# Kernel optimization log

Hardware: AMD Instinct MI355X
Metric: run time of the kernel (lower is better)

The kernel has to match this reference:

```python
import jax, jax.numpy as jnp
import numpy as np
import math

NUM_HEADS = 4
NUM_GROUPS = 16
EPS = 1e-5


def setup_inputs() -> dict:
    key = jax.random.key(0)
    ks = jax.random.split(key, 4)
    C = 256
    x = jax.random.normal(ks[0], (1, C, 16, 16, 16), dtype=jnp.float32)
    gn_gamma = jnp.ones((C,), dtype=jnp.float32)
    gn_beta = jnp.zeros((C,), dtype=jnp.float32)
    # conv3d 1x1 kernels == plain matrices [out_ch, in_ch]
    w_qkv = jax.random.normal(ks[1], (3 * C, C), dtype=jnp.float32) * (1.0 / math.sqrt(C))
    w_proj = jax.random.normal(ks[2], (C, C), dtype=jnp.float32) * (1.0 / math.sqrt(C))
    b_proj = jnp.zeros((C,), dtype=jnp.float32)
    return {"x": x, "gn_gamma": gn_gamma, "gn_beta": gn_beta,
            "w_qkv": w_qkv, "w_proj": w_proj, "b_proj": b_proj}


def reference(x, gn_gamma, gn_beta, w_qkv, w_proj, b_proj):
    B, C, H, W, D = x.shape
    N = H * W * D
    heads = NUM_HEADS
    d = C // heads

    xf = x.reshape(B, C, N)  # [B, C, N]

    # GroupNorm(16, C) with affine params
    xg = xf.reshape(B, NUM_GROUPS, C // NUM_GROUPS, N)
    mu = jnp.mean(xg, axis=(2, 3), keepdims=True)
    var = jnp.var(xg, axis=(2, 3), keepdims=True)
    xn = ((xg - mu) * jax.lax.rsqrt(var + EPS)).reshape(B, C, N)
    xn = xn * gn_gamma[None, :, None] + gn_beta[None, :, None]

    # 1x1 conv QKV: [B, 3C, N]
    qkv = jnp.einsum('oc,bcn->bon', w_qkv, xn)
    # torch: qkv.reshape(B*heads, 3d, N).chunk(3, dim=1)
    qkv = qkv.reshape(B * heads, 3 * d, N)
    q, k, v = qkv[:, :d], qkv[:, d:2 * d], qkv[:, 2 * d:]

    scale = 1.0 / math.sqrt(math.sqrt(d))
    attn = jnp.einsum('bct,bcs->bts', q * scale, k * scale)  # [B*heads, N, N]
    attn = jax.nn.softmax(attn, axis=-1)
    h = jnp.einsum('bts,bcs->bct', attn, v)  # [B*heads, d, N]

    h = h.reshape(B, C, N)
    out = jnp.einsum('oc,bcn->bon', w_proj, h) + b_proj[None, :, None]
    return (out + xf).reshape(B, C, H, W, D)
```

## Files before the change

kernel.cpp:

```cpp
#include <hip/hip_runtime.h>
#include <math.h>

#define N_TOK 4096
#define C_CH  256
#define SPLITS 4

typedef short bf16x8 __attribute__((ext_vector_type(8)));
typedef float f32x4  __attribute__((ext_vector_type(4)));
typedef unsigned short u16;

__device__ __forceinline__ u16 f2bf(float f) {
    union { float f; unsigned u; } v; v.f = f;
    unsigned r = v.u + 0x7FFF + ((v.u >> 16) & 1);
    return (u16)(r >> 16);
}
__device__ __forceinline__ float bf2f(u16 b) {
    union { unsigned u; float f; } v; v.u = ((unsigned)b) << 16;
    return v.f;
}
__device__ __forceinline__ unsigned packtr(float a, float b) {
    union { float f; unsigned u; } ua, ub; ua.f = a; ub.f = b;
    return __builtin_amdgcn_perm(ub.u, ua.u, 0x07060302u);
}

__global__ __launch_bounds__(256) void prep(const float* __restrict__ wqkv,
                                            const float* __restrict__ wproj,
                                            const float* __restrict__ x,
                                            u16* __restrict__ wq, u16* __restrict__ wp,
                                            float2* __restrict__ part) {
    __shared__ float rs[4], rss[4];
    if (blockIdx.x < 1024) {
        int i = blockIdx.x * 256 + threadIdx.x;
        if (i < 196608) {
            int row = i >> 8;
            float s = ((row % 192) < 64) ? 0.18033688f : 1.0f;
            wq[i] = f2bf(wqkv[i] * s);
        } else {
            wp[i - 196608] = f2bf(wproj[i - 196608]);
        }
    } else {
        const int b = blockIdx.x - 1024, tid = threadIdx.x;
        const int lane = tid & 63, wave = tid >> 6;
        const float4* xp = (const float4*)x + b * 1024;
        float s = 0.f, ss = 0.f;
#pragma unroll
        for (int k = 0; k < 4; ++k) {
            float4 v = xp[tid + k * 256];
            s  += v.x + v.y + v.z + v.w;
            ss += v.x * v.x + v.y * v.y + v.z * v.z + v.w * v.w;
        }
#pragma unroll
        for (int off = 1; off < 64; off <<= 1) {
            s  += __shfl_xor(s, off, 64);
            ss += __shfl_xor(ss, off, 64);
        }
        if (lane == 0) { rs[wave] = s; rss[wave] = ss; }
        __syncthreads();
        if (tid == 0) part[b] = make_float2(rs[0]+rs[1]+rs[2]+rs[3], rss[0]+rss[1]+rss[2]+rss[3]);
    }
}

__global__ __launch_bounds__(256) void qkv_gemm(const u16* __restrict__ wq,
                                                const float* __restrict__ x,
                                                const float2* __restrict__ part,
                                                const float* __restrict__ gamma,
                                                const float* __restrict__ beta,
                                                u16* __restrict__ QT,
                                                u16* __restrict__ KTm,
                                                u16* __restrict__ Vc) {
    const int nb = blockIdx.x * 64;
    const int tid = threadIdx.x;
    const int wave = tid >> 6, lane = tid & 63;
    const int quad = lane >> 4, low = lane & 15;
    const int mo = blockIdx.y * 64 + wave * 16;

    __shared__ __align__(16) u16 Xs[64 * 256];
    __shared__ float sca[256], scb[256];

    {
        const int ch = tid, g = ch >> 4;
        float s = 0.f, ss = 0.f;
#pragma unroll
        for (int j = 0; j < 16; ++j) { float2 p = part[g * 16 + j]; s += p.x; ss += p.y; }
        float mu = s * (1.f / 65536.f);
        float var = ss * (1.f / 65536.f) - mu * mu;
        float a = rsqrtf(var + 1e-5f) * gamma[ch];
        sca[ch] = a; scb[ch] = beta[ch] - mu * a;
    }
    __syncthreads();

#pragma unroll
    for (int i = 0; i < 8; ++i) {
        const int g = wave * 8 + i;
        u16 pk[8];
#pragma unroll
        for (int j = 0; j < 8; ++j) {
            const int ch = g * 8 + j;
            pk[j] = f2bf(x[ch * N_TOK + nb + lane] * sca[ch] + scb[ch]);
        }
        *(uint4*)(Xs + lane * 256 + ((g ^ (lane & 7)) * 8)) = *(const uint4*)pk;
    }
    __syncthreads();

    f32x4 acc[4] = {f32x4{0,0,0,0}, f32x4{0,0,0,0}, f32x4{0,0,0,0}, f32x4{0,0,0,0}};
#pragma unroll
    for (int kc = 0; kc < 8; ++kc) {
        bf16x8 af = *(const bf16x8*)(wq + (mo + low) * 256 + kc * 32 + quad * 8);
#pragma unroll
        for (int nt = 0; nt < 4; ++nt) {
            bf16x8 bf_ = *(const bf16x8*)(Xs + (nt * 16 + low) * 256 +
                                          (((kc * 4 + quad) ^ (low & 7)) * 8));
            acc[nt] = __builtin_amdgcn_mfma_f32_16x16x32_bf16(af, bf_, acc[nt], 0, 0, 0);
        }
    }

    const int kind = blockIdx.y % 3;
    const int head = blockIdx.y / 3;
    const int crow = wave * 16 + quad * 4;

    if (kind < 2) {
        u16* dst = (kind == 0 ? QT : KTm) + head * (N_TOK * 64);
#pragma unroll
        for (int nt = 0; nt < 4; ++nt) {
            int tok = nb + nt * 16 + low;
            u16 q4[4];
#pragma unroll
            for (int r = 0; r < 4; ++r) q4[r] = f2bf(acc[nt][r]);
            *(uint2*)(dst + tok * 64 + crow) = *(const uint2*)q4;
        }
    } else {
        __syncthreads();
        u16* Ts = Xs;
#pragma unroll
        for (int nt = 0; nt < 4; ++nt) {
            int tokl = nt * 16 + low;
#pragma unroll
            for (int r = 0; r < 4; ++r)
                Ts[(crow + r) * 72 + tokl] = f2bf(acc[nt][r]);
        }
        __syncthreads();
        u16* dst = Vc + head * (64 * N_TOK) + nb;
#pragma unroll
        for (int i = 0; i < 2; ++i) {
            int idx = i * 256 + tid;
            int c = idx >> 3, ch = idx & 7;
            uint4 v = *(const uint4*)(Ts + c * 72 + ch * 8);
            *(uint4*)(dst + c * N_TOK + ch * 8) = v;
        }
    }
}

__global__ __launch_bounds__(256, 2) void attn_kernel(const u16* __restrict__ QT,
                                                      const u16* __restrict__ KTm,
                                                      const u16* __restrict__ Vc,
                                                      u16* __restrict__ Op,
                                                      float* __restrict__ Lp) {
    const int head = blockIdx.y, split = blockIdx.z;
    const int qb   = blockIdx.x * 128;
    const int tid  = threadIdx.x;
    const int wave = tid >> 6, lane = tid & 63;
    const int quad = lane >> 4, low = lane & 15;

    const u16* Qh = QT  + head * N_TOK * 64;
    const u16* Kh = KTm + head * N_TOK * 64 + split * 1024 * 64;
    const u16* Vh = Vc  + head * 64 * N_TOK + split * 1024;

    __shared__ u16 Ks[2][64 * 64];
    __shared__ u16 Vs[2][64 * 64];
    __shared__ u16 Ps[4 * 32 * 64];
    u16* Pw = Ps + wave * 2048;

    bf16x8 ones;
#pragma unroll
    for (int i = 0; i < 8; ++i) ones[i] = (short)0x3F80;

    bf16x8 bq[2][2];
#pragma unroll
    for (int tn = 0; tn < 2; ++tn)
#pragma unroll
        for (int kh = 0; kh < 2; ++kh)
            bq[tn][kh] = *(const bf16x8*)(Qh + (qb + wave * 32 + tn * 16 + low) * 64 + kh * 32 + quad * 8);

    f32x4 oa[2][4], lC[2];
#pragma unroll
    for (int mt = 0; mt < 2; ++mt) {
        lC[mt] = f32x4{0,0,0,0};
#pragma unroll
        for (int cn = 0; cn < 4; ++cn) oa[mt][cn] = f32x4{0,0,0,0};
    }

    const int sA = tid >> 3, gA = tid & 7;
    const int swA = ((gA ^ (sA & 7)) * 8);
    const int swB = ((gA ^ ((sA + 32) & 7)) * 8);
    uint4 pk0 = *(const uint4*)(Kh + sA * 64 + gA * 8);
    uint4 pk1 = *(const uint4*)(Kh + (sA + 32) * 64 + gA * 8);
    uint4 pv0 = *(const uint4*)(Vh + sA * N_TOK + gA * 8);
    uint4 pv1 = *(const uint4*)(Vh + (sA + 32) * N_TOK + gA * 8);
    *(uint4*)(Ks[0] + sA * 64 + swA) = pk0;
    *(uint4*)(Ks[0] + (sA + 32) * 64 + swB) = pk1;
    *(uint4*)(Vs[0] + sA * 64 + swA) = pv0;
    *(uint4*)(Vs[0] + (sA + 32) * 64 + swB) = pv1;
    pk0 = *(const uint4*)(Kh + (64 + sA) * 64 + gA * 8);
    pk1 = *(const uint4*)(Kh + (64 + sA + 32) * 64 + gA * 8);
    pv0 = *(const uint4*)(Vh + sA * N_TOK + 64 + gA * 8);
    pv1 = *(const uint4*)(Vh + (sA + 32) * N_TOK + 64 + gA * 8);

    const int low7 = low & 7;

    for (int kt = 0; kt < 16; ++kt) {
        const int cur = kt & 1;
        const u16* Kc = Ks[cur];
        const u16* Vu = Vs[cur];
        __syncthreads();
        if (kt < 15) {
            u16* Kn = Ks[cur ^ 1]; u16* Vn = Vs[cur ^ 1];
            *(uint4*)(Kn + sA * 64 + swA) = pk0;
            *(uint4*)(Kn + (sA + 32) * 64 + swB) = pk1;
            *(uint4*)(Vn + sA * 64 + swA) = pv0;
            *(uint4*)(Vn + (sA + 32) * 64 + swB) = pv1;
            if (kt < 14) {
                int sb2 = (kt + 2) * 64;
                pk0 = *(const uint4*)(Kh + (sb2 + sA) * 64 + gA * 8);
                pk1 = *(const uint4*)(Kh + (sb2 + sA + 32) * 64 + gA * 8);
                pv0 = *(const uint4*)(Vh + sA * N_TOK + sb2 + gA * 8);
                pv1 = *(const uint4*)(Vh + (sA + 32) * N_TOK + sb2 + gA * 8);
            }
        }

        f32x4 sa[4][2];
#pragma unroll
        for (int sm = 0; sm < 4; ++sm)
#pragma unroll
            for (int tn = 0; tn < 2; ++tn) sa[sm][tn] = f32x4{0,0,0,0};
#pragma unroll
        for (int kh = 0; kh < 2; ++kh)
#pragma unroll
            for (int sm = 0; sm < 4; ++sm) {
                bf16x8 ak = *(const bf16x8*)(Kc + (sm * 16 + low) * 64 + (((quad + 4 * kh) ^ low7) * 8));
#pragma unroll
                for (int tn = 0; tn < 2; ++tn)
                    sa[sm][tn] = __builtin_amdgcn_mfma_f32_16x16x32_bf16(ak, bq[tn][kh], sa[sm][tn], 0, 0, 0);
            }

#pragma unroll
        for (int sm = 0; sm < 4; ++sm)
#pragma unroll
            for (int tn = 0; tn < 2; ++tn) {
                float p0 = exp2f(sa[sm][tn][0]);
                float p1 = exp2f(sa[sm][tn][1]);
                float p2 = exp2f(sa[sm][tn][2]);
                float p3 = exp2f(sa[sm][tn][3]);
                uint2 pk; pk.x = packtr(p0, p1); pk.y = packtr(p2, p3);
                int t = tn * 16 + low;
                int sw = ((sm * 2 + (quad >> 1)) ^ low7);
                *(uint2*)(Pw + t * 64 + sw * 8 + (quad & 1) * 4) = pk;
            }
        asm volatile("s_waitcnt lgkmcnt(0)" ::: "memory");

#pragma unroll
        for (int kh = 0; kh < 2; ++kh) {
            bf16x8 ap0 = *(const bf16x8*)(Pw + (low) * 64      + (((quad + 4 * kh) ^ low7) * 8));
            bf16x8 ap1 = *(const bf16x8*)(Pw + (16 + low) * 64 + (((quad + 4 * kh) ^ low7) * 8));
            lC[0] = __builtin_amdgcn_mfma_f32_16x16x32_bf16(ap0, ones, lC[0], 0, 0, 0);
            lC[1] = __builtin_amdgcn_mfma_f32_16x16x32_bf16(ap1, ones, lC[1], 0, 0, 0);
#pragma unroll
            for (int cn = 0; cn < 4; ++cn) {
                bf16x8 bv = *(const bf16x8*)(Vu + (cn * 16 + low) * 64 + (((quad + 4 * kh) ^ low7) * 8));
                oa[0][cn] = __builtin_amdgcn_mfma_f32_16x16x32_bf16(ap0, bv, oa[0][cn], 0, 0, 0);
                oa[1][cn] = __builtin_amdgcn_mfma_f32_16x16x32_bf16(ap1, bv, oa[1][cn], 0, 0, 0);
            }
        }
    }

    const int sh = (split * 4 + head) * N_TOK;
#pragma unroll
    for (int mt = 0; mt < 2; ++mt)
#pragma unroll
        for (int r = 0; r < 4; ++r) {
            int t = qb + wave * 32 + mt * 16 + quad * 4 + r;
            if (low == 0) Lp[sh + t] = lC[mt][r];
#pragma unroll
            for (int cn = 0; cn < 4; ++cn)
                Op[(sh + t) * 64 + cn * 16 + low] = f2bf(oa[mt][cn][r]);
        }
}

__global__ __launch_bounds__(256) void proj_gemm(const u16* __restrict__ wp,
                                                 const u16* __restrict__ Op,
                                                 const float* __restrict__ Lp,
                                                 const float* __restrict__ bias,
                                                 const float* __restrict__ xres,
                                                 float* __restrict__ out) {
    const int nb = blockIdx.x * 32;
    const int mo = blockIdx.y * 128 + (threadIdx.x >> 6) * 32;
    const int lane = threadIdx.x & 63;
    const int quad = lane >> 4, low = lane & 15;

    __shared__ u16 hT[32 * 264];

#pragma unroll
    for (int i = 0; i < 4; ++i) {
        int idx = i * 256 + threadIdx.x;
        int t = idx >> 5, cc = idx & 31;
        int head = cc >> 3;
        int tok = nb + t;
        float l = 0.f;
        float o[8] = {0.f,0.f,0.f,0.f,0.f,0.f,0.f,0.f};
#pragma unroll
        for (int sp = 0; sp < SPLITS; ++sp) {
            int b = (sp * 4 + head) * N_TOK + tok;
            l += Lp[b];
            uint4 pv = *(const uint4*)(Op + b * 64 + (cc & 7) * 8);
            const u16* ps = (const u16*)&pv;
#pragma unroll
            for (int j = 0; j < 8; ++j) o[j] += bf2f(ps[j]);
        }
        float rl = 1.f / l;
        u16 res[8];
#pragma unroll
        for (int j = 0; j < 8; ++j) res[j] = f2bf(o[j] * rl);
        *(uint4*)(hT + t * 264 + cc * 8) = *(const uint4*)res;
    }
    __syncthreads();

    f32x4 acc[2][2] = {{f32x4{0,0,0,0}, f32x4{0,0,0,0}}, {f32x4{0,0,0,0}, f32x4{0,0,0,0}}};
#pragma unroll
    for (int kc = 0; kc < 8; ++kc) {
#pragma unroll
        for (int mt = 0; mt < 2; ++mt) {
            bf16x8 af = *(const bf16x8*)(wp + (mo + mt * 16 + low) * 256 + kc * 32 + quad * 8);
#pragma unroll
            for (int nt = 0; nt < 2; ++nt) {
                bf16x8 bf_ = *(const bf16x8*)(hT + (nt * 16 + low) * 264 + kc * 32 + quad * 8);
                acc[mt][nt] = __builtin_amdgcn_mfma_f32_16x16x32_bf16(af, bf_, acc[mt][nt], 0, 0, 0);
            }
        }
    }
#pragma unroll
    for (int mt = 0; mt < 2; ++mt)
#pragma unroll
        for (int r = 0; r < 4; ++r) {
            int o = mo + mt * 16 + quad * 4 + r;
            float bv = bias[o];
#pragma unroll
            for (int nt = 0; nt < 2; ++nt) {
                int tok = nb + nt * 16 + low;
                out[o * N_TOK + tok] = acc[mt][nt][r] + bv + xres[o * N_TOK + tok];
            }
        }
}

extern "C" void kernel_launch(void* const* d_in, const int* in_sizes, int n_in,
                              void* d_out, int out_size, void* d_ws, size_t ws_size,
                              hipStream_t stream) {
    const float* x      = (const float*)d_in[0];
    const float* gamma  = (const float*)d_in[1];
    const float* beta   = (const float*)d_in[2];
    const float* w_qkv  = (const float*)d_in[3];
    const float* w_proj = (const float*)d_in[4];
    const float* b_proj = (const float*)d_in[5];
    float* out = (float*)d_out;

    char* base = (char*)d_ws;
    u16*    Op    = (u16*)base;
    float*  Lp    = (float*)(base + 8388608);
    float2* part  = (float2*)(base + 8654848);
    u16*    wq    = (u16*)(base + 8658944);
    u16*    wp    = (u16*)(base + 9052160);
    u16*    QT    = (u16*)(base + 9183232);
    u16*    KTm   = (u16*)(base + 11280384);
    u16*    Vc    = (u16*)(base + 13377536);

    prep      <<<1280, 256, 0, stream>>>(w_qkv, w_proj, x, wq, wp, part);
    qkv_gemm  <<<dim3(64, 12), 256, 0, stream>>>(wq, x, part, gamma, beta, QT, KTm, Vc);
    attn_kernel<<<dim3(32, 4, SPLITS), 256, 0, stream>>>(QT, KTm, Vc, Op, Lp);
    proj_gemm <<<dim3(128, 2), 256, 0, stream>>>(wp, Op, Lp, b_proj, x, out);
}
```

Baseline: 118.4 us.

## Stage attention output through LDS for coalesced stores; widen proj_gemm tiles

The attention kernel now writes its per-wave output tile into a swizzled shared-memory buffer (Pw) and then copies it to global memory as 16-byte rows, replacing scattered 2-byte stores. The projection GEMM now covers all 256 output channels per block, with each wave handling 64 rows, so the split-K combine of partial attention outputs is done once per token block instead of twice. This cuts uncoalesced global writes and redundant reduction work, but the proj grid shrinks to 128 blocks and each thread holds more accumulators. Pw is not declared in the visible hunk, and the LDS round-trip relies only on an lgkmcnt wait with no barrier, which is only safe if each wave reads back rows it wrote itself.

```diff
diff --git a/kernel.cpp b/kernel.cpp
--- a/kernel.cpp
+++ b/kernel.cpp
@@ -279,10 +279,29 @@
         for (int r = 0; r < 4; ++r) {
             int t = qb + wave * 32 + mt * 16 + quad * 4 + r;
             if (low == 0) Lp[sh + t] = lC[mt][r];
-#pragma unroll
-            for (int cn = 0; cn < 4; ++cn)
-                Op[(sh + t) * 64 + cn * 16 + low] = f2bf(oa[mt][cn][r]);
-        }
+        }
+#pragma unroll
+    for (int mt = 0; mt < 2; ++mt)
+#pragma unroll
+        for (int cn = 0; cn < 4; ++cn) {
+            int c = cn * 16 + low;
+            int chunk = c >> 3, cl = c & 7;
+#pragma unroll
+            for (int r = 0; r < 4; ++r) {
+                int tr = mt * 16 + quad * 4 + r;
+                Pw[tr * 64 + ((chunk ^ (tr & 7)) * 8) + cl] = f2bf(oa[mt][cn][r]);
+            }
+        }
+    asm volatile("s_waitcnt lgkmcnt(0)" ::: "memory");
+    {
+        const int r8 = lane >> 3, ch = lane & 7;
+#pragma unroll
+        for (int it = 0; it < 4; ++it) {
+            int row = it * 8 + r8;
+            uint4 v = *(const uint4*)(Pw + row * 64 + ((ch ^ (row & 7)) * 8));
+            *(uint4*)(Op + (sh + qb + wave * 32 + row) * 64 + ch * 8) = v;
+        }
+    }
 }
 
 __global__ __launch_bounds__(256) void proj_gemm(const u16* __restrict__ wp,
@@ -292,7 +311,7 @@
                                                  const float* __restrict__ xres,
                                                  float* __restrict__ out) {
     const int nb = blockIdx.x * 32;
-    const int mo = blockIdx.y * 128 + (threadIdx.x >> 6) * 32;
+    const int mo = (threadIdx.x >> 6) * 64;
     const int lane = threadIdx.x & 63;
     const int quad = lane >> 4, low = lane & 15;
 
@@ -323,21 +342,21 @@
     }
     __syncthreads();
 
-    f32x4 acc[2][2] = {{f32x4{0,0,0,0}, f32x4{0,0,0,0}}, {f32x4{0,0,0,0}, f32x4{0,0,0,0}}};
+    f32x4 acc[4][2] = {{f32x4{0,0,0,0}, f32x4{0,0,0,0}}, {f32x4{0,0,0,0}, f32x4{0,0,0,0}},
+                       {f32x4{0,0,0,0}, f32x4{0,0,0,0}}, {f32x4{0,0,0,0}, f32x4{0,0,0,0}}};
 #pragma unroll
     for (int kc = 0; kc < 8; ++kc) {
-#pragma unroll
-        for (int mt = 0; mt < 2; ++mt) {
+        bf16x8 b0 = *(const bf16x8*)(hT + (low) * 264      + kc * 32 + quad * 8);
+        bf16x8 b1 = *(const bf16x8*)(hT + (16 + low) * 264 + kc * 32 + quad * 8);
+#pragma unroll
+        for (int mt = 0; mt < 4; ++mt) {
             bf16x8 af = *(const bf16x8*)(wp + (mo + mt * 16 + low) * 256 + kc * 32 + quad * 8);
-#pragma unroll
-            for (int nt = 0; nt < 2; ++nt) {
-                bf16x8 bf_ = *(const bf16x8*)(hT + (nt * 16 + low) * 264 + kc * 32 + quad * 8);
-                acc[mt][nt] = __builtin_amdgcn_mfma_f32_16x16x32_bf16(af, bf_, acc[mt][nt], 0, 0, 0);
-            }
-        }
-    }
-#pragma unroll
-    for (int mt = 0; mt < 2; ++mt)
+            acc[mt][0] = __builtin_amdgcn_mfma_f32_16x16x32_bf16(af, b0, acc[mt][0], 0, 0, 0);
+            acc[mt][1] = __builtin_amdgcn_mfma_f32_16x16x32_bf16(af, b1, acc[mt][1], 0, 0, 0);
+        }
+    }
+#pragma unroll
+    for (int mt = 0; mt < 4; ++mt)
 #pragma unroll
         for (int r = 0; r < 4; ++r) {
             int o = mo + mt * 16 + quad * 4 + r;
@@ -374,5 +393,5 @@
     prep      <<<1280, 256, 0, stream>>>(w_qkv, w_proj, x, wq, wp, part);
     qkv_gemm  <<<dim3(64, 12), 256, 0, stream>>>(wq, x, part, gamma, beta, QT, KTm, Vc);
     attn_kernel<<<dim3(32, 4, SPLITS), 256, 0, stream>>>(QT, KTm, Vc, Op, Lp);
-    proj_gemm <<<dim3(128, 2), 256, 0, stream>>>(wp, Op, Lp, b_proj, x, out);
-}
+    proj_gemm <<<128, 256, 0, stream>>>(wp, Op, Lp, b_proj, x, out);
+}
```

After: 124.9 us. +5.5%, slower.
